# Kernel tuning notes

Measured on AMD Instinct MI355X. Metric: run time of the kernel, lower is better.

Reference implementation:

```python
import jax, jax.numpy as jnp
import numpy as np

L = 2        # n_layer
D = 1024     # hidden_size
H = 8        # n_head
DK = D // H  # head_dim = 128
DV = D // H
T = 2048     # max_seq_length
B = 4
INTER = 2816 # fla GatedMLP: int(1024*4*2/3)=2730 rounded up to multiple of 256
EPS = 1e-6


def rmsnorm(x, w):
    return x * jax.lax.rsqrt(jnp.mean(x * x, axis=-1, keepdims=True) + EPS) * w


def l2norm(x):
    return x * jax.lax.rsqrt(jnp.sum(x * x, axis=-1, keepdims=True) + EPS)


def delta_attn(x, Wq, Wk, Wv, Wb, Wo, onorm_w):
    # x: [B, T, D]
    b, t, _ = x.shape
    q = jax.nn.silu((x @ Wq).reshape(b, t, H, DK))
    k = jax.nn.silu((x @ Wk).reshape(b, t, H, DK))
    q = l2norm(q)
    k = l2norm(k)
    v = jax.nn.silu((x @ Wv).reshape(b, t, H, DV))
    beta = jax.nn.sigmoid(x @ Wb) * 2.0  # [B,T,H], allow_neg_eigval=True
    # time-major for scan
    qt = q.transpose(1, 0, 2, 3)  # [T,B,H,DK]
    kt = k.transpose(1, 0, 2, 3)
    vt = v.transpose(1, 0, 2, 3)
    bt = beta.transpose(1, 0, 2)  # [T,B,H]

    def step(S, inps):
        qi, ki, vi, bi = inps
        # delta rule: S_t = S_{t-1} + beta_t * k_t (v_t - S_{t-1}^T k_t)^T
        pred = jnp.einsum('bhkv,bhk->bhv', S, ki)
        S = S + bi[..., None, None] * ki[..., :, None] * (vi - pred)[..., None, :]
        o = jnp.einsum('bhkv,bhk->bhv', S, qi)
        return S, o

    S0 = jnp.zeros((b, H, DK, DV), x.dtype)
    _, o = jax.lax.scan(step, S0, (qt, kt, vt, bt))  # o: [T,B,H,DV]
    o = rmsnorm(o, onorm_w)  # per-head RMSNorm (use_gate=False)
    o = o.transpose(1, 0, 2, 3).reshape(b, t, H * DV)
    return o @ Wo


def setup_inputs() -> dict:
    key = jax.random.key(0)
    ks = jax.random.split(key, 13)
    s = 0.02
    f32 = jnp.float32
    return {
        'input_embeds': jax.random.normal(ks[0], (T, B, D), f32),
        'Wq': jax.random.normal(ks[1], (L, D, D), f32) * s,
        'Wk': jax.random.normal(ks[2], (L, D, D), f32) * s,
        'Wv': jax.random.normal(ks[3], (L, D, D), f32) * s,
        'Wb': jax.random.normal(ks[4], (L, D, H), f32) * s,
        'Wo': jax.random.normal(ks[5], (L, D, D), f32) * s,
        'onorm_w': jnp.ones((L, DV), f32) + jax.random.normal(ks[6], (L, DV), f32) * 0.02,
        'norm1_w': jnp.ones((L, D), f32) + jax.random.normal(ks[7], (L, D), f32) * 0.02,
        'norm2_w': jnp.ones((L, D), f32) + jax.random.normal(ks[8], (L, D), f32) * 0.02,
        'Wg': jax.random.normal(ks[9], (L, D, 2 * INTER), f32) * s,
        'Wd': jax.random.normal(ks[10], (L, INTER, D), f32) * s,
        'final_norm_w': jnp.ones((D,), f32) + jax.random.normal(ks[11], (D,), f32) * 0.02,
    }


def reference(input_embeds, Wq, Wk, Wv, Wb, Wo, onorm_w, norm1_w, norm2_w, Wg, Wd, final_norm_w):
    # wrapper transposes (T,B,D) -> (B,T,D)
    x = input_embeds.transpose(1, 0, 2)
    for l in range(L):
        h = rmsnorm(x, norm1_w[l])
        x = x + delta_attn(h, Wq[l], Wk[l], Wv[l], Wb[l], Wo[l], onorm_w[l])
        h = rmsnorm(x, norm2_w[l])
        gy = h @ Wg[l]
        g, y = jnp.split(gy, 2, axis=-1)
        x = x + (jax.nn.silu(g) * y) @ Wd[l]
    x = rmsnorm(x, final_norm_w)
    return x.transpose(1, 0, 2)  # back to (T,B,D)
```

## Files before the change

### kernel.cpp

```cpp
#include <hip/hip_runtime.h>
#include <hip/hip_bf16.h>
#include <cstdint>


typedef _Float16 f16;
typedef __attribute__((ext_vector_type(8))) _Float16 h8;
typedef __attribute__((ext_vector_type(4))) _Float16 h4;
typedef __attribute__((ext_vector_type(4))) float f4;

#define DEV __device__ __forceinline__

static constexpr int Bb_ = 4;
static constexpr int Hh  = 8;
static constexpr int Dd  = 1024;
static constexpr int Tt  = 2048;
static constexpr int NC  = 32;

DEV float siluf(float x) { return x / (1.f + expf(-x)); }
DEV int swz16(int row, int c) { return (c & 8) | ((c & 7) ^ (row & 7)); }

#define AS1(p) ((const __attribute__((address_space(1))) void*)(uintptr_t)(p))
#define AS3(p) ((__attribute__((address_space(3))) void*)(uint32_t)(uintptr_t)(p))

DEV void stage_half(const f16* __restrict__ srcRowBase, int K, int kt,
                    f16* dstHalf, int tid) {
#pragma unroll
  for (int i = 0; i < 2; ++i) {
    const int q = i * 512 + tid;
    const int r = q >> 3, cs = q & 7;
    const int cl = cs ^ (r & 7);
    __builtin_amdgcn_global_load_lds(AS1(srcRowBase + (size_t)r * K + kt * 64 + cl * 8),
                                     AS3(dstHalf + q * 8), 16, 0, 0);
  }
}
DEV h8 rd_sw(const f16* T, int row, int chunk) {
  return *(const h8*)(T + (((row << 3) | (chunk ^ (row & 7))) * 8));
}

template<int EPI, int BN>
__global__ __launch_bounds__(512, 2) void gemm2(const f16* __restrict__ A, const f16* __restrict__ Bt,
                                                void* __restrict__ C, const f16* __restrict__ Yp,
                                                int M, int N, int K, int gx) {
  constexpr int NCF = BN / 64;
  __shared__ __align__(16) f16 ldsA[2][16384];
  __shared__ __align__(16) f16 ldsB[2][BN * 64];
  const int tid = threadIdx.x, lane = tid & 63, w = tid >> 6;
  const int l15 = lane & 15, l4 = lane >> 4;
  const int wr = w >> 2, wc = w & 3;
  const int nwg = gridDim.x;
  int flat = blockIdx.x;
  if ((nwg & 7) == 0) flat = (flat & 7) * (nwg >> 3) + (flat >> 3);
  const int bx = flat % gx, by = flat / gx;

  const f16* Ab = A + (size_t)by * 256 * K;
  const f16* Bb = Bt + (size_t)bx * BN * K;
  const int NT = K >> 6;
  f4 acc[8][NCF] = {};

  stage_half(Bb, K, 0, ldsB[0], tid);
  if (BN == 256) stage_half(Bb + (size_t)128 * K, K, 0, ldsB[0] + 8192, tid);
  stage_half(Ab, K, 0, ldsA[0], tid);
  stage_half(Ab + (size_t)128 * K, K, 0, ldsA[0] + 8192, tid);
  if (NT > 1) {
    stage_half(Bb, K, 1, ldsB[1], tid);
    if (BN == 256) stage_half(Bb + (size_t)128 * K, K, 1, ldsB[1] + 8192, tid);
    if (BN == 256) asm volatile("s_waitcnt vmcnt(4)");
    else           asm volatile("s_waitcnt vmcnt(2)");
  } else {
    asm volatile("s_waitcnt vmcnt(0)");
  }
  __builtin_amdgcn_s_barrier();

  for (int t = 0; t < NT; ++t) {
    const int cur = t & 1, nxt = cur ^ 1;
    const f16* cA = ldsA[cur];
    const f16* cB = ldsB[cur];
    h8 b[NCF][2];
    h8 a[2][2];
#pragma unroll
    for (int cf = 0; cf < NCF; ++cf)
#pragma unroll
      for (int ks = 0; ks < 2; ++ks)
        b[cf][ks] = rd_sw(cB, wc * (BN / 4) + cf * 16 + l15, ks * 4 + l4);
#pragma unroll
    for (int fr = 0; fr < 2; ++fr)
#pragma unroll
      for (int ks = 0; ks < 2; ++ks)
        a[fr][ks] = rd_sw(cA, wr * 128 + fr * 16 + l15, ks * 4 + l4);
    if (t + 1 < NT) stage_half(Ab, K, t + 1, ldsA[nxt], tid);
    __builtin_amdgcn_s_barrier();
    asm volatile("s_waitcnt lgkmcnt(0)");
    __builtin_amdgcn_s_setprio(1);
#pragma unroll
    for (int fr = 0; fr < 2; ++fr)
#pragma unroll
      for (int cf = 0; cf < NCF; ++cf)
#pragma unroll
        for (int ks = 0; ks < 2; ++ks)
          acc[fr][cf] = __builtin_amdgcn_mfma_f32_16x16x32_f16(a[fr][ks], b[cf][ks], acc[fr][cf], 0, 0, 0);
    __builtin_amdgcn_s_setprio(0);
    __builtin_amdgcn_s_barrier();
#pragma unroll
    for (int p = 1; p < 4; ++p) {
#pragma unroll
      for (int fr = 0; fr < 2; ++fr)
#pragma unroll
        for (int ks = 0; ks < 2; ++ks)
          a[fr][ks] = rd_sw(cA, wr * 128 + p * 32 + fr * 16 + l15, ks * 4 + l4);
      if (p == 1 && t + 1 < NT) stage_half(Ab + (size_t)128 * K, K, t + 1, ldsA[nxt] + 8192, tid);
      if (p == 2 && t + 2 < NT) stage_half(Bb, K, t + 2, ldsB[cur], tid);
      if (BN == 256 && p == 3 && t + 2 < NT) stage_half(Bb + (size_t)128 * K, K, t + 2, ldsB[cur] + 8192, tid);
      __builtin_amdgcn_s_barrier();
      asm volatile("s_waitcnt lgkmcnt(0)");
      __builtin_amdgcn_s_setprio(1);
#pragma unroll
      for (int fr = 0; fr < 2; ++fr)
#pragma unroll
        for (int cf = 0; cf < NCF; ++cf)
#pragma unroll
          for (int ks = 0; ks < 2; ++ks)
            acc[p * 2 + fr][cf] = __builtin_amdgcn_mfma_f32_16x16x32_f16(a[fr][ks], b[cf][ks], acc[p * 2 + fr][cf], 0, 0, 0);
      __builtin_amdgcn_s_setprio(0);
      if (p == 3) {
        if (t + 2 < NT) {
          if (BN == 256) asm volatile("s_waitcnt vmcnt(4)");
          else           asm volatile("s_waitcnt vmcnt(2)");
        } else if (t + 1 < NT) {
          asm volatile("s_waitcnt vmcnt(0)");
        }
      }
      __builtin_amdgcn_s_barrier();
    }
  }

#pragma unroll
  for (int fr = 0; fr < 8; ++fr) {
#pragma unroll
    for (int cf = 0; cf < NCF; ++cf) {
      const int row0 = by * 256 + wr * 128 + fr * 16 + l4 * 4;
      const int col = bx * BN + wc * (BN / 4) + cf * 16 + l15;
#pragma unroll
      for (int q = 0; q < 4; ++q) {
        const size_t idx = (size_t)(row0 + q) * N + col;
        const float v = acc[fr][cf][q];
        if (EPI == 0) ((float*)C)[idx] = v;
        if (EPI == 1) ((f16*)C)[idx] = (f16)((float)((f16*)C)[idx] + v);
        if (EPI == 2) ((f16*)C)[idx] = (f16)v;
        if (EPI == 3) ((f16*)C)[idx] = (f16)(siluf(v) * (float)Yp[idx]);
      }
    }
  }
}

__global__ __launch_bounds__(256) void cvt_k(const float* __restrict__ in, f16* __restrict__ out) {
  const size_t i = ((size_t)blockIdx.x * 256 + threadIdx.x) * 8;
  const float4 a = *(const float4*)(in + i);
  const float4 b = *(const float4*)(in + i + 4);
  h8 o = {(f16)a.x, (f16)a.y, (f16)a.z, (f16)a.w, (f16)b.x, (f16)b.y, (f16)b.z, (f16)b.w};
  *(h8*)(out + i) = o;
}

template<int OUT_F16>
__global__ __launch_bounds__(256) void rmsnorm_k(const f16* __restrict__ x, const float* __restrict__ w,
                                                 void* __restrict__ out) {
  const int r = blockIdx.x, tid = threadIdx.x;
  const h4 xv = *(const h4*)(x + (size_t)r * 1024 + tid * 4);
  const float v0 = (float)xv[0], v1 = (float)xv[1], v2 = (float)xv[2], v3 = (float)xv[3];
  float ss = v0 * v0 + v1 * v1 + v2 * v2 + v3 * v3;
#pragma unroll
  for (int m = 1; m < 64; m <<= 1) ss += __shfl_xor(ss, m);
  __shared__ float red[4];
  if ((tid & 63) == 0) red[tid >> 6] = ss;
  __syncthreads();
  const float scale = rsqrtf((red[0] + red[1] + red[2] + red[3]) * (1.f / 1024.f) + 1e-6f);
  const float4 w4 = *(const float4*)(w + tid * 4);
  float o0 = v0 * scale * w4.x, o1 = v1 * scale * w4.y, o2 = v2 * scale * w4.z, o3 = v3 * scale * w4.w;
  if (OUT_F16) {
    h4 o = {(f16)o0, (f16)o1, (f16)o2, (f16)o3};
    *(h4*)((f16*)out + (size_t)r * 1024 + tid * 4) = o;
  } else {
    *(float4*)((float*)out + (size_t)r * 1024 + tid * 4) = make_float4(o0, o1, o2, o3);
  }
}

__global__ __launch_bounds__(256) void qkv_epi(const f16* __restrict__ qkv, f16* __restrict__ qb,
                                               f16* __restrict__ kb, f16* __restrict__ vb) {
  const int r = blockIdx.x, tid = threadIdx.x;
  const int head = tid >> 5, l32 = tid & 31;
  const int i = (r >> 2) & 63;
  const size_t src = (size_t)r * 3072 + head * 128 + l32 * 4;
  {
    const h4 v = *(const h4*)(qkv + src);
    float s0 = siluf((float)v[0]), s1 = siluf((float)v[1]), s2 = siluf((float)v[2]), s3 = siluf((float)v[3]);
    float ss = s0 * s0 + s1 * s1 + s2 * s2 + s3 * s3;
#pragma unroll
    for (int m = 1; m <= 16; m <<= 1) ss += __shfl_xor(ss, m);
    const float sc = rsqrtf(ss + 1e-6f);
    h4 o = {(f16)(s0 * sc), (f16)(s1 * sc), (f16)(s2 * sc), (f16)(s3 * sc)};
    const int c = l32 >> 1, off = (l32 & 1) * 4;
    *(h4*)(qb + (size_t)r * 1024 + head * 128 + swz16(i, c) * 8 + off) = o;
  }
  {
    const h4 v = *(const h4*)(qkv + src + 1024);
    float s0 = siluf((float)v[0]), s1 = siluf((float)v[1]), s2 = siluf((float)v[2]), s3 = siluf((float)v[3]);
    float ss = s0 * s0 + s1 * s1 + s2 * s2 + s3 * s3;
#pragma unroll
    for (int m = 1; m <= 16; m <<= 1) ss += __shfl_xor(ss, m);
    const float sc = rsqrtf(ss + 1e-6f);
    h4 o = {(f16)(s0 * sc), (f16)(s1 * sc), (f16)(s2 * sc), (f16)(s3 * sc)};
    const int c = l32 >> 1, off = (l32 & 1) * 4;
    *(h4*)(kb + (size_t)r * 1024 + head * 128 + swz16(i, c) * 8 + off) = o;
  }
  {
    const h4 v = *(const h4*)(qkv + (size_t)r * 3072 + 2048 + tid * 4);
    h4 o = {(f16)siluf((float)v[0]), (f16)siluf((float)v[1]), (f16)siluf((float)v[2]), (f16)siluf((float)v[3])};
    const int hd = tid >> 5, dh = (tid & 31) * 4;
    const int c = dh >> 3, off = dh & 7;
    *(h4*)(vb + (size_t)r * 1024 + hd * 128 + swz16(i, c) * 8 + off) = o;
  }
}

__global__ __launch_bounds__(256) void onorm_k(const f16* __restrict__ o, const float* __restrict__ w,
                                               f16* __restrict__ ob) {
  const int r = blockIdx.x, tid = threadIdx.x;
  const int head = tid >> 5, l32 = tid & 31;
  const size_t base = (size_t)r * 1024 + head * 128 + l32 * 4;
  const h4 xv = *(const h4*)(o + base);
  const float v0 = (float)xv[0], v1 = (float)xv[1], v2 = (float)xv[2], v3 = (float)xv[3];
  float ss = v0 * v0 + v1 * v1 + v2 * v2 + v3 * v3;
#pragma unroll
  for (int m = 1; m <= 16; m <<= 1) ss += __shfl_xor(ss, m);
  const float sc = rsqrtf(ss * (1.f / 128.f) + 1e-6f);
  const float4 w4 = *(const float4*)(w + l32 * 4);
  h4 out = {(f16)(v0 * sc * w4.x), (f16)(v1 * sc * w4.y), (f16)(v2 * sc * w4.z), (f16)(v3 * sc * w4.w)};
  *(h4*)(ob + base) = out;
}

__global__ __launch_bounds__(256) void beta_k(const f16* __restrict__ hb, const float* __restrict__ Wb,
                                              float* __restrict__ beta) {
  const int tid = threadIdx.x, lane = tid & 63, wv = tid >> 6;
  const int r = blockIdx.x * 4 + wv;
  const f16* row = hb + (size_t)r * 1024 + lane * 16;
  const h8 v0 = *(const h8*)(row);
  const h8 v1 = *(const h8*)(row + 8);
  const float* wb = Wb + (size_t)(lane * 16) * 8;
  float acc[8] = {};
#pragma unroll
  for (int e = 0; e < 8; ++e) {
    const float x0 = (float)v0[e], x1 = (float)v1[e];
    const float4 w0a = *(const float4*)(wb + e * 8);
    const float4 w0b = *(const float4*)(wb + e * 8 + 4);
    const float4 w1a = *(const float4*)(wb + (e + 8) * 8);
    const float4 w1b = *(const float4*)(wb + (e + 8) * 8 + 4);
    acc[0] += x0 * w0a.x + x1 * w1a.x;  acc[1] += x0 * w0a.y + x1 * w1a.y;
    acc[2] += x0 * w0a.z + x1 * w1a.z;  acc[3] += x0 * w0a.w + x1 * w1a.w;
    acc[4] += x0 * w0b.x + x1 * w1b.x;  acc[5] += x0 * w0b.y + x1 * w1b.y;
    acc[6] += x0 * w0b.z + x1 * w1b.z;  acc[7] += x0 * w0b.w + x1 * w1b.w;
  }
#pragma unroll
  for (int j = 0; j < 8; ++j)
#pragma unroll
    for (int m = 1; m < 64; m <<= 1) acc[j] += __shfl_xor(acc[j], m);
  if (lane == 0) {
#pragma unroll
    for (int j = 0; j < 8; ++j) beta[(size_t)r * 8 + j] = 2.f / (1.f + expf(-acc[j]));
  }
}

__global__ __launch_bounds__(256) void transpose_k(const float* __restrict__ W, f16* __restrict__ Wt,
                                                   int K, int N) {
  __shared__ float tile[32][33];
  const int n0 = blockIdx.x * 32, k0 = blockIdx.y * 32;
  const int tx = threadIdx.x & 31, ty = threadIdx.x >> 5;
#pragma unroll
  for (int i = 0; i < 32; i += 8) tile[ty + i][tx] = W[(size_t)(k0 + ty + i) * N + n0 + tx];
  __syncthreads();
#pragma unroll
  for (int i = 0; i < 32; i += 8) Wt[(size_t)(n0 + ty + i) * K + k0 + tx] = (f16)tile[tx][ty + i];
}

__global__ void fill_k(float* p, int n, float v) {
  const int i = blockIdx.x * 256 + threadIdx.x;
  if (i < n) p[i] = v;
}

DEV f4 mm16(const f16* A, int as, const f16* B, f4 c, int l15, int l4) {
  h4 a = *(const h4*)(A + l15 * as + l4 * 4);
  h4 b = *(const h4*)(B + l15 * 20 + l4 * 4);
  return __builtin_amdgcn_mfma_f32_16x16x16f16(a, b, c, 0, 0, 0);
}
DEV void wr_T(f16* slot, f4 acc, int l15, int l4, float sgn) {
  h4 v = {(f16)(sgn * acc[0]), (f16)(sgn * acc[1]), (f16)(sgn * acc[2]), (f16)(sgn * acc[3])};
  *(h4*)(slot + l15 * 20 + l4 * 4) = v;
}
DEV void wr_Tb(f16* Tb, int bi, int bj, f4 acc, const float* betas, int l15, int l4, float sgn) {
  const float bc = betas[bj * 16 + l15];
#pragma unroll
  for (int q = 0; q < 4; ++q)
    Tb[(bi * 16 + l4 * 4 + q) * 72 + bj * 16 + l15] = (f16)(sgn * acc[q] * bc);
}

__global__ __launch_bounds__(256) void phaseA(const f16* __restrict__ kb, const f16* __restrict__ qb,
                                              const f16* __restrict__ vb, const float* __restrict__ beta,
                                              f16* __restrict__ wbuf, f16* __restrict__ utbuf,
                                              f16* __restrict__ pbuf, f16* __restrict__ ktbuf) {
  const int blk = blockIdx.x;
  const int c = blk >> 5, bh = blk & 31;
  const int b = bh >> 3, h = bh & 7;
  const int tid = threadIdx.x, lane = tid & 63, wv = tid >> 6;
  const int l15 = lane & 15, l4 = lane >> 4;

  __shared__ __align__(16) f16 Ks[64 * 128];
  __shared__ __align__(16) f16 QVs[64 * 128];
  __shared__ __align__(16) f16 Abuf[64 * 68];
  __shared__ __align__(16) f16 Dr[4][16 * 20];
  __shared__ __align__(16) f16 Dt[4][16 * 20];
  __shared__ __align__(16) f16 Tp[3][16 * 20];
  __shared__ __align__(16) f16 Xp[3][16 * 20];
  __shared__ __align__(16) f16 Tb[64 * 72];
  __shared__ float betas[64];

  const size_t rowstr = (size_t)Bb_ * Dd;
  const size_t gbase = ((size_t)(c * 64) * Bb_ + b) * Dd + h * 128;

#pragma unroll
  for (int i = 0; i < 4; ++i) {
    const int ch = tid + i * 256;
    const int rr = ch >> 4, kc = ch & 15;
    *(h8*)(Ks + ch * 8) = *(const h8*)(kb + gbase + (size_t)rr * rowstr + kc * 8);
    *(h8*)(QVs + ch * 8) = *(const h8*)(qb + gbase + (size_t)rr * rowstr + kc * 8);
  }
  for (int i = tid; i < 64 * 72; i += 256) Tb[i] = (f16)0.f;
  if (tid < 64) betas[tid] = beta[((size_t)(c * 64 + tid) * Bb_ + b) * Hh + h];
  __syncthreads();

  f4 accS[4] = {}, accP[4] = {};
  const int arow = wv * 16 + l15;
#pragma unroll
  for (int kc = 0; kc < 4; ++kc) {
    const int c4 = kc * 4 + l4;
    const h8 aK = *(const h8*)(Ks + arow * 128 + swz16(arow, c4) * 8);
    const h8 aQ = *(const h8*)(QVs + arow * 128 + swz16(arow, c4) * 8);
#pragma unroll
    for (int f = 0; f < 4; ++f) {
      const int brow = f * 16 + l15;
      const h8 bK = *(const h8*)(Ks + brow * 128 + swz16(brow, c4) * 8);
      accS[f] = __builtin_amdgcn_mfma_f32_16x16x32_f16(aK, bK, accS[f], 0, 0, 0);
      accP[f] = __builtin_amdgcn_mfma_f32_16x16x32_f16(aQ, bK, accP[f], 0, 0, 0);
    }
  }
  const size_t pbase = (((size_t)bh * NC + c) * 64) * 64;
#pragma unroll
  for (int f = 0; f < 4; ++f) {
#pragma unroll
    for (int q = 0; q < 4; ++q) {
      const int i = wv * 16 + l4 * 4 + q;
      const int j = f * 16 + l15;
      Abuf[i * 68 + j] = (f16)((j < i) ? betas[i] * accS[f][q] : 0.f);
      pbuf[pbase + (size_t)i * 64 + j] = (f16)((j <= i) ? accP[f][q] : 0.f);
    }
  }
  __syncthreads();

#pragma unroll
  for (int i = 0; i < 4; ++i) {
    const int ch = tid + i * 256;
    const int rr = ch >> 4, kc = ch & 15;
    *(h8*)(QVs + ch * 8) = *(const h8*)(vb + gbase + (size_t)rr * rowstr + kc * 8);
  }

  {
    const int bi = wv;
    const int cc = l15;
    const f16* Ad = Abuf + (bi * 16) * 68 + bi * 16;
    float t[16];
    t[0] = (cc == 0) ? 1.f : 0.f;
#pragma unroll
    for (int i = 1; i < 16; ++i) {
      float s = (cc == i) ? 1.f : 0.f;
#pragma unroll
      for (int j = 0; j < i; ++j) s -= (float)Ad[i * 68 + j] * t[j];
      t[i] = s;
    }
    if (lane < 16) {
#pragma unroll
      for (int j4 = 0; j4 < 4; ++j4) {
        h4 v = {(f16)t[j4 * 4], (f16)t[j4 * 4 + 1], (f16)t[j4 * 4 + 2], (f16)t[j4 * 4 + 3]};
        *(h4*)(&Dt[bi][cc * 20 + j4 * 4]) = v;
      }
      const float bc = betas[bi * 16 + cc];
#pragma unroll
      for (int j = 0; j < 16; ++j) {
        Dr[bi][j * 20 + cc] = (f16)t[j];
        Tb[(bi * 16 + j) * 72 + bi * 16 + cc] = (f16)(t[j] * bc);
      }
    }
  }
  __syncthreads();

  const f16* AB10 = Abuf + 16 * 68 + 0;
  const f16* AB20 = Abuf + 32 * 68 + 0;
  const f16* AB21 = Abuf + 32 * 68 + 16;
  const f16* AB30 = Abuf + 48 * 68 + 0;
  const f16* AB31 = Abuf + 48 * 68 + 16;
  const f16* AB32 = Abuf + 48 * 68 + 32;
  f4 z = {};
  f4 x20, x30;

  if (wv == 0) wr_T(Xp[0], mm16(AB10, 68, Dt[0], z, l15, l4), l15, l4, 1.f);
  if (wv == 1) wr_T(Xp[1], mm16(AB21, 68, Dt[1], z, l15, l4), l15, l4, 1.f);
  if (wv == 2) wr_T(Xp[2], mm16(AB32, 68, Dt[2], z, l15, l4), l15, l4, 1.f);
  if (wv == 3) x20 = mm16(AB20, 68, Dt[0], z, l15, l4);
  __syncthreads();
  if (wv == 0) { f4 r = mm16(Dr[1], 20, Xp[0], z, l15, l4); wr_T(Tp[0], r, l15, l4, -1.f); wr_Tb(Tb, 1, 0, r, betas, l15, l4, -1.f); }
  if (wv == 1) { f4 r = mm16(Dr[2], 20, Xp[1], z, l15, l4); wr_T(Tp[1], r, l15, l4, -1.f); wr_Tb(Tb, 2, 1, r, betas, l15, l4, -1.f); }
  if (wv == 2) { f4 r = mm16(Dr[3], 20, Xp[2], z, l15, l4); wr_Tb(Tb, 3, 2, r, betas, l15, l4, -1.f); }
  if (wv == 3) x30 = mm16(AB30, 68, Dt[0], z, l15, l4);
  __syncthreads();
  if (wv == 3) wr_T(Xp[0], mm16(AB21, 68, Tp[0], x20, l15, l4), l15, l4, 1.f);
  if (wv == 1) { f4 r = mm16(AB31, 68, Dt[1], z, l15, l4); r = mm16(AB32, 68, Tp[1], r, l15, l4); wr_T(Xp[1], r, l15, l4, 1.f); }
  __syncthreads();
  if (wv == 3) { f4 r = mm16(Dr[2], 20, Xp[0], z, l15, l4); wr_T(Tp[2], r, l15, l4, -1.f); wr_Tb(Tb, 2, 0, r, betas, l15, l4, -1.f); }
  if (wv == 1) { f4 r = mm16(Dr[3], 20, Xp[1], z, l15, l4); wr_Tb(Tb, 3, 1, r, betas, l15, l4, -1.f); }
  __syncthreads();
  if (wv == 3) { f4 r = mm16(AB31, 68, Tp[0], x30, l15, l4); r = mm16(AB32, 68, Tp[2], r, l15, l4); wr_T(Xp[2], r, l15, l4, 1.f); }
  __syncthreads();
  if (wv == 3) { f4 r = mm16(Dr[3], 20, Xp[2], z, l15, l4); wr_Tb(Tb, 3, 0, r, betas, l15, l4, -1.f); }
  __syncthreads();

  const size_t wub = ((size_t)bh * NC + c) * 8192;
  const int koff = l4 * 8;
  f4 wacc[8] = {}, uacc[8] = {};
#pragma unroll
  for (int kc = 0; kc < 2; ++kc) {
    const h8 aT = *(const h8*)(Tb + (wv * 16 + l15) * 72 + kc * 32 + koff);
#pragma unroll
    for (int f = 0; f < 8; ++f) {
      const int d = f * 16 + l15, cD = d >> 3, d7 = d & 7;
      h8 bK, bV;
#pragma unroll
      for (int j = 0; j < 8; ++j) {
        const int t2 = kc * 32 + koff + j;
        const int pos = t2 * 128 + swz16(t2, cD) * 8 + d7;
        bK[j] = Ks[pos];
        bV[j] = QVs[pos];
      }
      wacc[f] = __builtin_amdgcn_mfma_f32_16x16x32_f16(aT, bK, wacc[f], 0, 0, 0);
      uacc[f] = __builtin_amdgcn_mfma_f32_16x16x32_f16(aT, bV, uacc[f], 0, 0, 0);
    }
  }
#pragma unroll
  for (int f = 0; f < 8; ++f) {
    const int d = f * 16 + l15, cD = d >> 3, d7 = d & 7;
#pragma unroll
    for (int q = 0; q < 4; ++q) {
      const int i = wv * 16 + l4 * 4 + q;
      wbuf[wub + (size_t)i * 128 + swz16(i, cD) * 8 + d7] = (f16)wacc[f][q];
    }
    h4 uv = {(f16)uacc[f][0], (f16)uacc[f][1], (f16)uacc[f][2], (f16)uacc[f][3]};
    *(h4*)(utbuf + wub + (size_t)d * 64 + wv * 16 + l4 * 4) = uv;
  }

#pragma unroll
  for (int i2 = 0; i2 < 4; ++i2) {
    const int ch = tid + i2 * 256;
    const int dp = ch & 127, c2 = ch >> 7;
    h8 v;
#pragma unroll
    for (int j = 0; j < 8; ++j) {
      const int i = c2 * 8 + j;
      v[j] = Ks[i * 128 + swz16(i, dp >> 3) * 8 + (dp & 7)];
    }
    *(h8*)(ktbuf + wub + (size_t)dp * 64 + (c2 ^ (dp & 7)) * 8) = v;
  }
}

__global__ __launch_bounds__(256) void phaseB(const f16* __restrict__ qb, const f16* __restrict__ ktbuf,
                                              const f16* __restrict__ wbuf, const f16* __restrict__ utbuf,
                                              const f16* __restrict__ pbuf, f16* __restrict__ obuf) {
  const int blk = blockIdx.x;
  const int bh = blk >> 2, g = blk & 3;
  const int b = bh >> 3, h = bh & 7;
  const int tid = threadIdx.x, lane = tid & 63, wv = tid >> 6;
  const int l15 = lane & 15, l4 = lane >> 4;

  __shared__ __align__(16) f16 Ws[2][8192];
  __shared__ __align__(16) f16 Qs[2][8192];
  __shared__ __align__(16) f16 Kts[2][8192];
  __shared__ __align__(16) f16 Rt[32 * 72];
  __shared__ __align__(16) f16 Ms[32 * 136];

  for (int i = tid; i < 32 * 136; i += 256) Ms[i] = (f16)0.f;
  f4 macc[2][2] = {};

  const int arow = wv * 16 + l15;
  const int koff = l4 * 8;

  auto STAGE = [&](int c2, int buf) {
#pragma unroll
    for (int i = 0; i < 4; ++i) {
      const int ch = tid + i * 256;
      const size_t tb = ((size_t)bh * NC + c2) * 8192;
      __builtin_amdgcn_global_load_lds(AS1(wbuf + tb + ch * 8), AS3(Ws[buf] + ch * 8), 16, 0, 0);
      __builtin_amdgcn_global_load_lds(AS1(ktbuf + tb + ch * 8), AS3(Kts[buf] + ch * 8), 16, 0, 0);
      const int rr = ch >> 4, kc2 = ch & 15;
      __builtin_amdgcn_global_load_lds(AS1(qb + ((size_t)((c2 * 64 + rr) * 4 + b)) * 1024 + h * 128 + kc2 * 8),
                                       AS3(Qs[buf] + ch * 8), 16, 0, 0);
    }
  };

  STAGE(0, 0);
  asm volatile("s_waitcnt vmcnt(0)" ::: "memory");
  __builtin_amdgcn_s_barrier();

  for (int c = 0; c < NC; ++c) {
    const int cur = c & 1, nxt = cur ^ 1;
    const size_t pcb = ((size_t)bh * NC + c) * 4096;
    const h8 aP0 = *(const h8*)(pbuf + pcb + arow * 64 + koff);
    const h8 aP1 = *(const h8*)(pbuf + pcb + arow * 64 + 32 + koff);
    const size_t ucb = ((size_t)bh * NC + c) * 8192;
    const h4 u0 = *(const h4*)(utbuf + ucb + (size_t)(g * 32 + l15) * 64 + wv * 16 + l4 * 4);
    const h4 u1 = *(const h4*)(utbuf + ucb + (size_t)(g * 32 + 16 + l15) * 64 + wv * 16 + l4 * 4);
    asm volatile("s_waitcnt vmcnt(4)" ::: "memory");
    asm volatile("s_waitcnt lgkmcnt(0)" ::: "memory");
    __builtin_amdgcn_s_barrier();
    if (c + 1 < NC) STAGE(c + 1, nxt);

    f4 accR[2] = {}, accO[2] = {};
    __builtin_amdgcn_s_setprio(1);
#pragma unroll
    for (int kc = 0; kc < 4; ++kc) {
      const int c4 = kc * 4 + l4;
      const h8 aW = *(const h8*)(Ws[cur] + arow * 128 + swz16(arow, c4) * 8);
      const h8 aQ = *(const h8*)(Qs[cur] + arow * 128 + swz16(arow, c4) * 8);
#pragma unroll
      for (int f = 0; f < 2; ++f) {
        const h8 bM = *(const h8*)(Ms + (f * 16 + l15) * 136 + kc * 32 + koff);
        accR[f] = __builtin_amdgcn_mfma_f32_16x16x32_f16(aW, bM, accR[f], 0, 0, 0);
        accO[f] = __builtin_amdgcn_mfma_f32_16x16x32_f16(aQ, bM, accO[f], 0, 0, 0);
      }
    }
    __builtin_amdgcn_s_setprio(0);
    if (c + 1 < NC) asm volatile("s_waitcnt vmcnt(12)" ::: "memory");
    else            asm volatile("s_waitcnt vmcnt(0)" ::: "memory");
#pragma unroll
    for (int f = 0; f < 2; ++f) {
      const h4 uu = f ? u1 : u0;
      h4 rw;
#pragma unroll
      for (int q = 0; q < 4; ++q) {
        const float rv = (float)uu[q] - accR[f][q];
        accR[f][q] = rv;
        rw[q] = (f16)rv;
      }
      *(h4*)(Rt + (f * 16 + l15) * 72 + wv * 16 + l4 * 4) = rw;
    }
    asm volatile("s_waitcnt lgkmcnt(0)" ::: "memory");
    __builtin_amdgcn_s_barrier();

#pragma unroll
    for (int kc = 0; kc < 2; ++kc) {
      const h8 aP = kc ? aP1 : aP0;
#pragma unroll
      for (int f = 0; f < 2; ++f) {
        const h8 bR = *(const h8*)(Rt + (f * 16 + l15) * 72 + kc * 32 + koff);
        accO[f] = __builtin_amdgcn_mfma_f32_16x16x32_f16(aP, bR, accO[f], 0, 0, 0);
      }
    }
#pragma unroll
    for (int f = 0; f < 2; ++f)
#pragma unroll
      for (int q = 0; q < 4; ++q) {
        const int i = wv * 16 + l4 * 4 + q;
        const int cc = f * 16 + l15;
        obuf[((size_t)(c * 64 + i) * Bb_ + b) * Dd + h * 128 + g * 32 + cc] = (f16)accO[f][q];
      }

#pragma unroll
    for (int kc = 0; kc < 2; ++kc) {
      const h8 aR0 = *(const h8*)(Rt + l15 * 72 + kc * 32 + koff);
      const h8 aR1 = *(const h8*)(Rt + (16 + l15) * 72 + kc * 32 + koff);
#pragma unroll
      for (int cf = 0; cf < 2; ++cf) {
        const int kcol = wv * 32 + cf * 16 + l15;
        const int c2 = kc * 4 + l4;
        const h8 bKv = *(const h8*)(Kts[cur] + kcol * 64 + (c2 ^ (kcol & 7)) * 8);
        macc[0][cf] = __builtin_amdgcn_mfma_f32_16x16x32_f16(aR0, bKv, macc[0][cf], 0, 0, 0);
        macc[1][cf] = __builtin_amdgcn_mfma_f32_16x16x32_f16(aR1, bKv, macc[1][cf], 0, 0, 0);
      }
    }
#pragma unroll
    for (int rf = 0; rf < 2; ++rf)
#pragma unroll
      for (int cf = 0; cf < 2; ++cf)
#pragma unroll
        for (int q = 0; q < 4; ++q) {
          const int cr = rf * 16 + l4 * 4 + q;
          const int kcol = wv * 32 + cf * 16 + l15;
          Ms[cr * 136 + kcol] = (f16)macc[rf][cf][q];
        }
  }
}

extern "C" void kernel_launch(void* const* d_in, const int* in_sizes, int n_in,
                              void* d_out, int out_size, void* d_ws, size_t ws_size,
                              hipStream_t stream) {
  (void)in_sizes; (void)n_in;
  const float* input = (const float*)d_in[0];
  const float* Wq = (const float*)d_in[1];
  const float* Wk = (const float*)d_in[2];
  const float* Wv = (const float*)d_in[3];
  const float* Wb = (const float*)d_in[4];
  const float* Wo = (const float*)d_in[5];
  const float* onw = (const float*)d_in[6];
  const float* n1w = (const float*)d_in[7];
  const float* n2w = (const float*)d_in[8];
  const float* Wg = (const float*)d_in[9];
  const float* Wd = (const float*)d_in[10];
  const float* fnw = (const float*)d_in[11];

  char* ws = (char*)d_ws;
  size_t off = 0;
  auto alloc = [&](size_t bytes) { void* p = ws + off; off += (bytes + 255) & ~(size_t)255; return p; };
  const size_t RD = 8192ull * 1024ull;
  f16*  x     = (f16*)alloc(RD * 2);
  f16*  hb    = (f16*)alloc(RD * 2);
  f16*  qb    = (f16*)alloc(RD * 2);
  f16*  kbuf  = (f16*)alloc(RD * 2);
  f16*  vbuf  = (f16*)alloc(RD * 2);
  float* beta = (float*)alloc(8192ull * 8 * 4);
  f16*  wbuf  = (f16*)alloc(RD * 2);
  f16*  utbuf = (f16*)alloc(RD * 2);
  f16*  ktbuf = (f16*)alloc(RD * 2);
  f16*  pbuf  = (f16*)alloc(32ull * 32 * 64 * 64 * 2);
  char* arena = (char*)alloc(3 * RD * 2);
  f16*  WqkvT = (f16*)alloc(3072ull * 1024 * 2);
  f16*  WoT   = (f16*)alloc(1024ull * 1024 * 2);
  f16*  WgT   = (f16*)alloc(5632ull * 1024 * 2);
  f16*  WdT   = (f16*)alloc(1024ull * 2816 * 2);
  if (off > ws_size) {
    fill_k<<<(out_size + 255) / 256, 256, 0, stream>>>((float*)d_out, out_size, 1.0e6f);
    return;
  }
  f16* qkvraw = (f16*)arena;
  f16* obuf = (f16*)arena;
  f16* Ybuf = (f16*)arena;
  f16* my = qb;
  f16* ob = wbuf;

  cvt_k<<<4096, 256, 0, stream>>>(input, x);

  for (int l = 0; l < 2; ++l) {
    const size_t o2 = (size_t)l * 1024 * 1024;
    transpose_k<<<dim3(32, 32), 256, 0, stream>>>(Wq + o2, WqkvT, 1024, 1024);
    transpose_k<<<dim3(32, 32), 256, 0, stream>>>(Wk + o2, WqkvT + 1024ull * 1024, 1024, 1024);
    transpose_k<<<dim3(32, 32), 256, 0, stream>>>(Wv + o2, WqkvT + 2048ull * 1024, 1024, 1024);
    transpose_k<<<dim3(32, 32), 256, 0, stream>>>(Wo + o2, WoT, 1024, 1024);
    transpose_k<<<dim3(176, 32), 256, 0, stream>>>(Wg + (size_t)l * 1024 * 5632, WgT, 1024, 5632);
    transpose_k<<<dim3(32, 88), 256, 0, stream>>>(Wd + (size_t)l * 2816 * 1024, WdT, 2816, 1024);

    rmsnorm_k<1><<<8192, 256, 0, stream>>>(x, n1w + l * 1024, hb);
    gemm2<2, 256><<<32 * 12, 512, 0, stream>>>(hb, WqkvT, qkvraw, nullptr, 8192, 3072, 1024, 12);
    beta_k<<<2048, 256, 0, stream>>>(hb, Wb + (size_t)l * 1024 * 8, beta);
    qkv_epi<<<8192, 256, 0, stream>>>(qkvraw, qb, kbuf, vbuf);
    phaseA<<<1024, 256, 0, stream>>>(kbuf, qb, vbuf, beta, wbuf, utbuf, pbuf, ktbuf);
    phaseB<<<128, 256, 0, stream>>>(qb, ktbuf, wbuf, utbuf, pbuf, obuf);
    onorm_k<<<8192, 256, 0, stream>>>(obuf, onw + l * 128, ob);
    gemm2<1, 128><<<32 * 8, 512, 0, stream>>>(ob, WoT, x, nullptr, 8192, 1024, 1024, 8);

    rmsnorm_k<1><<<8192, 256, 0, stream>>>(x, n2w + l * 1024, hb);
    gemm2<2, 256><<<32 * 11, 512, 0, stream>>>(hb, WgT + 2816ull * 1024, Ybuf, nullptr, 8192, 2816, 1024, 11);
    gemm2<3, 256><<<32 * 11, 512, 0, stream>>>(hb, WgT, my, Ybuf, 8192, 2816, 1024, 11);
    gemm2<1, 128><<<32 * 8, 512, 0, stream>>>(my, WdT, x, nullptr, 8192, 1024, 2816, 8);
  }
  rmsnorm_k<0><<<8192, 256, 0, stream>>>(x, fnw, d_out);
}
```

Before: 1.064 ms.

## Fuse gate and up projections into one GLU GEMM and trim staging barriers

Adds a gemmGLU kernel that computes the gate and up projections together in one pass over the same A tiles. It applies silu(g)*y in the epilogue, so the separate Y buffer is never written to or read back from global memory. The GEMM staging now uses precomputed per-thread offsets through a lambda, and one barrier per sub-step is dropped, relying on double buffering for safety. The QKV GEMM switches from BN=256 to BN=128 with twice the workgroups. The fused kernel holds two accumulator sets, which raises register pressure and may lower occupancy.

```diff
diff --git a/kernel.cpp b/kernel.cpp
--- a/kernel.cpp
+++ b/kernel.cpp
@@ -22,26 +22,13 @@
 #define AS1(p) ((const __attribute__((address_space(1))) void*)(uintptr_t)(p))
 #define AS3(p) ((__attribute__((address_space(3))) void*)(uint32_t)(uintptr_t)(p))
 
-DEV void stage_half(const f16* __restrict__ srcRowBase, int K, int kt,
-                    f16* dstHalf, int tid) {
-#pragma unroll
-  for (int i = 0; i < 2; ++i) {
-    const int q = i * 512 + tid;
-    const int r = q >> 3, cs = q & 7;
-    const int cl = cs ^ (r & 7);
-    __builtin_amdgcn_global_load_lds(AS1(srcRowBase + (size_t)r * K + kt * 64 + cl * 8),
-                                     AS3(dstHalf + q * 8), 16, 0, 0);
-  }
-}
 DEV h8 rd_sw(const f16* T, int row, int chunk) {
   return *(const h8*)(T + (((row << 3) | (chunk ^ (row & 7))) * 8));
 }
 
 template<int EPI, int BN>
 __global__ __launch_bounds__(512, 2) void gemm2(const f16* __restrict__ A, const f16* __restrict__ Bt,
-                                                void* __restrict__ C, const f16* __restrict__ Yp,
-                                                int M, int N, int K, int gx) {
-  constexpr int NCF = BN / 64;
+                                                void* __restrict__ C, int M, int N, int K, int gx) {
   __shared__ __align__(16) f16 ldsA[2][16384];
   __shared__ __align__(16) f16 ldsB[2][BN * 64];
   const int tid = threadIdx.x, lane = tid & 63, w = tid >> 6;
@@ -55,15 +42,25 @@
   const f16* Ab = A + (size_t)by * 256 * K;
   const f16* Bb = Bt + (size_t)bx * BN * K;
   const int NT = K >> 6;
+  constexpr int NCF = BN / 64;
   f4 acc[8][NCF] = {};
 
-  stage_half(Bb, K, 0, ldsB[0], tid);
-  if (BN == 256) stage_half(Bb + (size_t)128 * K, K, 0, ldsB[0] + 8192, tid);
-  stage_half(Ab, K, 0, ldsA[0], tid);
-  stage_half(Ab + (size_t)128 * K, K, 0, ldsA[0] + 8192, tid);
+  const int r0 = tid >> 3;
+  const size_t soff0 = (size_t)r0 * K + (size_t)(((tid & 7) ^ (r0 & 7)) * 8);
+  const size_t soff1 = soff0 + (size_t)64 * K;
+  const int dof = tid * 8;
+  auto STG = [&](const f16* base, f16* dst) {
+    __builtin_amdgcn_global_load_lds(AS1(base + soff0), AS3(dst + dof), 16, 0, 0);
+    __builtin_amdgcn_global_load_lds(AS1(base + soff1), AS3(dst + 4096 + dof), 16, 0, 0);
+  };
+
+  STG(Bb, ldsB[0]);
+  if (BN == 256) STG(Bb + (size_t)128 * K, ldsB[0] + 8192);
+  STG(Ab, ldsA[0]);
+  STG(Ab + (size_t)128 * K, ldsA[0] + 8192);
   if (NT > 1) {
-    stage_half(Bb, K, 1, ldsB[1], tid);
-    if (BN == 256) stage_half(Bb + (size_t)128 * K, K, 1, ldsB[1] + 8192, tid);
+    STG(Bb + 64, ldsB[1]);
+    if (BN == 256) STG(Bb + (size_t)128 * K + 64, ldsB[1] + 8192);
     if (BN == 256) asm volatile("s_waitcnt vmcnt(4)");
     else           asm volatile("s_waitcnt vmcnt(2)");
   } else {
@@ -87,8 +84,7 @@
 #pragma unroll
       for (int ks = 0; ks < 2; ++ks)
         a[fr][ks] = rd_sw(cA, wr * 128 + fr * 16 + l15, ks * 4 + l4);
-    if (t + 1 < NT) stage_half(Ab, K, t + 1, ldsA[nxt], tid);
-    __builtin_amdgcn_s_barrier();
+    if (t + 1 < NT) STG(Ab + (t + 1) * 64, ldsA[nxt]);
     asm volatile("s_waitcnt lgkmcnt(0)");
     __builtin_amdgcn_s_setprio(1);
 #pragma unroll
@@ -107,10 +103,9 @@
 #pragma unroll
         for (int ks = 0; ks < 2; ++ks)
           a[fr][ks] = rd_sw(cA, wr * 128 + p * 32 + fr * 16 + l15, ks * 4 + l4);
-      if (p == 1 && t + 1 < NT) stage_half(Ab + (size_t)128 * K, K, t + 1, ldsA[nxt] + 8192, tid);
-      if (p == 2 && t + 2 < NT) stage_half(Bb, K, t + 2, ldsB[cur], tid);
-      if (BN == 256 && p == 3 && t + 2 < NT) stage_half(Bb + (size_t)128 * K, K, t + 2, ldsB[cur] + 8192, tid);
-      __builtin_amdgcn_s_barrier();
+      if (p == 1 && t + 1 < NT) STG(Ab + (size_t)128 * K + (t + 1) * 64, ldsA[nxt] + 8192);
+      if (p == 2 && t + 2 < NT) STG(Bb + (t + 2) * 64, ldsB[cur]);
+      if (BN == 256 && p == 3 && t + 2 < NT) STG(Bb + (size_t)128 * K + (t + 2) * 64, ldsB[cur] + 8192);
       asm volatile("s_waitcnt lgkmcnt(0)");
       __builtin_amdgcn_s_setprio(1);
 #pragma unroll
@@ -146,8 +141,122 @@
         if (EPI == 0) ((float*)C)[idx] = v;
         if (EPI == 1) ((f16*)C)[idx] = (f16)((float)((f16*)C)[idx] + v);
         if (EPI == 2) ((f16*)C)[idx] = (f16)v;
-        if (EPI == 3) ((f16*)C)[idx] = (f16)(siluf(v) * (float)Yp[idx]);
-      }
+      }
+    }
+  }
+}
+
+__global__ __launch_bounds__(512, 2) void gemmGLU(const f16* __restrict__ A, const f16* __restrict__ WgT,
+                                                  f16* __restrict__ my, int K, int gx) {
+  __shared__ __align__(16) f16 ldsA[2][16384];
+  __shared__ __align__(16) f16 ldsG[2][8192];
+  __shared__ __align__(16) f16 ldsY[2][8192];
+  const int tid = threadIdx.x, lane = tid & 63, w = tid >> 6;
+  const int l15 = lane & 15, l4 = lane >> 4;
+  const int wr = w >> 2, wc = w & 3;
+  const int nwg = gridDim.x;
+  int flat = blockIdx.x;
+  if ((nwg & 7) == 0) flat = (flat & 7) * (nwg >> 3) + (flat >> 3);
+  const int bx = flat % gx, by = flat / gx;
+
+  const f16* Ab = A + (size_t)by * 256 * K;
+  const f16* Gb = WgT + (size_t)bx * 128 * K;
+  const f16* Yb = WgT + (size_t)(2816 + bx * 128) * K;
+  const int NT = K >> 6;
+  f4 accG[8][2] = {}, accY[8][2] = {};
+
+  const int r0 = tid >> 3;
+  const size_t soff0 = (size_t)r0 * K + (size_t)(((tid & 7) ^ (r0 & 7)) * 8);
+  const size_t soff1 = soff0 + (size_t)64 * K;
+  const int dof = tid * 8;
+  auto STG = [&](const f16* base, f16* dst) {
+    __builtin_amdgcn_global_load_lds(AS1(base + soff0), AS3(dst + dof), 16, 0, 0);
+    __builtin_amdgcn_global_load_lds(AS1(base + soff1), AS3(dst + 4096 + dof), 16, 0, 0);
+  };
+
+  STG(Gb, ldsG[0]);
+  STG(Yb, ldsY[0]);
+  STG(Ab, ldsA[0]);
+  STG(Ab + (size_t)128 * K, ldsA[0] + 8192);
+  if (NT > 1) {
+    STG(Gb + 64, ldsG[1]);
+    STG(Yb + 64, ldsY[1]);
+    asm volatile("s_waitcnt vmcnt(4)");
+  } else {
+    asm volatile("s_waitcnt vmcnt(0)");
+  }
+  __builtin_amdgcn_s_barrier();
+
+  for (int t = 0; t < NT; ++t) {
+    const int cur = t & 1, nxt = cur ^ 1;
+    const f16* cA = ldsA[cur];
+    h8 bg[2][2], byv[2][2];
+    h8 a[2][2];
+#pragma unroll
+    for (int cf = 0; cf < 2; ++cf)
+#pragma unroll
+      for (int ks = 0; ks < 2; ++ks) {
+        bg[cf][ks] = rd_sw(ldsG[cur], wc * 32 + cf * 16 + l15, ks * 4 + l4);
+        byv[cf][ks] = rd_sw(ldsY[cur], wc * 32 + cf * 16 + l15, ks * 4 + l4);
+      }
+#pragma unroll
+    for (int fr = 0; fr < 2; ++fr)
+#pragma unroll
+      for (int ks = 0; ks < 2; ++ks)
+        a[fr][ks] = rd_sw(cA, wr * 128 + fr * 16 + l15, ks * 4 + l4);
+    if (t + 1 < NT) STG(Ab + (t + 1) * 64, ldsA[nxt]);
+    asm volatile("s_waitcnt lgkmcnt(0)");
+    __builtin_amdgcn_s_setprio(1);
+#pragma unroll
+    for (int fr = 0; fr < 2; ++fr)
+#pragma unroll
+      for (int cf = 0; cf < 2; ++cf)
+#pragma unroll
+        for (int ks = 0; ks < 2; ++ks) {
+          accG[fr][cf] = __builtin_amdgcn_mfma_f32_16x16x32_f16(a[fr][ks], bg[cf][ks], accG[fr][cf], 0, 0, 0);
+          accY[fr][cf] = __builtin_amdgcn_mfma_f32_16x16x32_f16(a[fr][ks], byv[cf][ks], accY[fr][cf], 0, 0, 0);
+        }
+    __builtin_amdgcn_s_setprio(0);
+    __builtin_amdgcn_s_barrier();
+#pragma unroll
+    for (int p = 1; p < 4; ++p) {
+#pragma unroll
+      for (int fr = 0; fr < 2; ++fr)
+#pragma unroll
+        for (int ks = 0; ks < 2; ++ks)
+          a[fr][ks] = rd_sw(cA, wr * 128 + p * 32 + fr * 16 + l15, ks * 4 + l4);
+      if (p == 1 && t + 1 < NT) STG(Ab + (size_t)128 * K + (t + 1) * 64, ldsA[nxt] + 8192);
+      if (p == 2 && t + 2 < NT) STG(Gb + (t + 2) * 64, ldsG[cur]);
+      if (p == 3 && t + 2 < NT) STG(Yb + (t + 2) * 64, ldsY[cur]);
+      asm volatile("s_waitcnt lgkmcnt(0)");
+      __builtin_amdgcn_s_setprio(1);
+#pragma unroll
+      for (int fr = 0; fr < 2; ++fr)
+#pragma unroll
+        for (int cf = 0; cf < 2; ++cf)
+#pragma unroll
+          for (int ks = 0; ks < 2; ++ks) {
+            accG[p * 2 + fr][cf] = __builtin_amdgcn_mfma_f32_16x16x32_f16(a[fr][ks], bg[cf][ks], accG[p * 2 + fr][cf], 0, 0, 0);
+            accY[p * 2 + fr][cf] = __builtin_amdgcn_mfma_f32_16x16x32_f16(a[fr][ks], byv[cf][ks], accY[p * 2 + fr][cf], 0, 0, 0);
+          }
+      __builtin_amdgcn_s_setprio(0);
+      if (p == 3) {
+        if (t + 2 < NT) asm volatile("s_waitcnt vmcnt(4)");
+        else if (t + 1 < NT) asm volatile("s_waitcnt vmcnt(0)");
+      }
+      __builtin_amdgcn_s_barrier();
+    }
+  }
+
+#pragma unroll
+  for (int fr = 0; fr < 8; ++fr) {
+#pragma unroll
+    for (int cf = 0; cf < 2; ++cf) {
+      const int row0 = by * 256 + wr * 128 + fr * 16 + l4 * 4;
+      const int col = bx * 128 + wc * 32 + cf * 16 + l15;
+#pragma unroll
+      for (int q = 0; q < 4; ++q)
+        my[(size_t)(row0 + q) * 2816 + col] = (f16)(siluf(accG[fr][cf][q]) * accY[fr][cf][q]);
     }
   }
 }
@@ -644,7 +753,6 @@
   }
   f16* qkvraw = (f16*)arena;
   f16* obuf = (f16*)arena;
-  f16* Ybuf = (f16*)arena;
   f16* my = qb;
   f16* ob = wbuf;
 
@@ -660,18 +768,17 @@
     transpose_k<<<dim3(32, 88), 256, 0, stream>>>(Wd + (size_t)l * 2816 * 1024, WdT, 2816, 1024);
 
     rmsnorm_k<1><<<8192, 256, 0, stream>>>(x, n1w + l * 1024, hb);
-    gemm2<2, 256><<<32 * 12, 512, 0, stream>>>(hb, WqkvT, qkvraw, nullptr, 8192, 3072, 1024, 12);
+    gemm2<2, 128><<<32 * 24, 512, 0, stream>>>(hb, WqkvT, qkvraw, 8192, 3072, 1024, 24);
     beta_k<<<2048, 256, 0, stream>>>(hb, Wb + (size_t)l * 1024 * 8, beta);
     qkv_epi<<<8192, 256, 0, stream>>>(qkvraw, qb, kbuf, vbuf);
     phaseA<<<1024, 256, 0, stream>>>(kbuf, qb, vbuf, beta, wbuf, utbuf, pbuf, ktbuf);
     phaseB<<<128, 256, 0, stream>>>(qb, ktbuf, wbuf, utbuf, pbuf, obuf);
     onorm_k<<<8192, 256, 0, stream>>>(obuf, onw + l * 128, ob);
-    gemm2<1, 128><<<32 * 8, 512, 0, stream>>>(ob, WoT, x, nullptr, 8192, 1024, 1024, 8);
+    gemm2<1, 128><<<32 * 8, 512, 0, stream>>>(ob, WoT, x, 8192, 1024, 1024, 8);
 
     rmsnorm_k<1><<<8192, 256, 0, stream>>>(x, n2w + l * 1024, hb);
-    gemm2<2, 256><<<32 * 11, 512, 0, stream>>>(hb, WgT + 2816ull * 1024, Ybuf, nullptr, 8192, 2816, 1024, 11);
-    gemm2<3, 256><<<32 * 11, 512, 0, stream>>>(hb, WgT, my, Ybuf, 8192, 2816, 1024, 11);
-    gemm2<1, 128><<<32 * 8, 512, 0, stream>>>(my, WdT, x, nullptr, 8192, 1024, 2816, 8);
+    gemmGLU<<<32 * 22, 512, 0, stream>>>(hb, WgT, my, 1024, 22);
+    gemm2<1, 128><<<32 * 8, 512, 0, stream>>>(my, WdT, x, 8192, 1024, 2816, 8);
   }
   rmsnorm_k<0><<<8192, 256, 0, stream>>>(x, fnw, d_out);
 }
```

After: 993.7 us. 6.6% less time.
